# Kernel tuning notes

Measured on AMD Instinct MI355X. Metric: run time of the kernel, lower is better.

## Reference

```python
import jax, jax.numpy as jnp
import numpy as np

NR_EMB = 1024
B_COMMITMENT = 1.0


def setup_inputs() -> dict:
    key = jax.random.key(0)
    k1, k2 = jax.random.split(key)
    inpt = jax.random.normal(k1, (64, 2048, 64), dtype=jnp.float32)
    # VarianceScaling(uniform) over shape (D, K): limit = sqrt(3*scale/fan_in), scale=1, fan_in=D
    D = 64
    limit = np.sqrt(3.0 / D).astype(np.float32)
    emb_mtrx = jax.random.uniform(k2, (D, NR_EMB), dtype=jnp.float32, minval=-limit, maxval=limit)
    return {"inpt": inpt, "emb_mtrx": emb_mtrx}


def reference(inpt, emb_mtrx):
    D = inpt.shape[-1]
    x = inpt.reshape(-1, D)  # [N, D]
    dist = (jnp.sum(x * x, axis=1, keepdims=True)
            - 2.0 * (x @ emb_mtrx)
            + jnp.sum(emb_mtrx * emb_mtrx, axis=0, keepdims=True))
    idx = jnp.argmax(-dist, axis=1)  # [N]
    # avg_probs = mean of one-hot over N == normalized histogram (same math, no N x K one-hot)
    avg_probs = jnp.bincount(idx, length=NR_EMB).astype(inpt.dtype) / x.shape[0]
    perplexity = jnp.exp(-jnp.sum(avg_probs * jnp.log(avg_probs + 1e-10)))
    idx_nd = idx.reshape(inpt.shape[:-1])  # [B, T]
    q = jnp.take(emb_mtrx.T, idx_nd, axis=0)  # gather codebook rows -> [B, T, D]
    l_commitment = jnp.mean((jax.lax.stop_gradient(q) - inpt) ** 2)
    l_codebook = jnp.mean((q - jax.lax.stop_gradient(inpt)) ** 2)
    loss = B_COMMITMENT * l_commitment + l_codebook
    q = inpt + jax.lax.stop_gradient(q - inpt)  # straight-through estimator
    return q, loss, perplexity
```

## Files before the change

kernel.cpp:

```cpp
#include <hip/hip_runtime.h>

#define NROWS 131072
#define D 64
#define K 1024

typedef __attribute__((ext_vector_type(8))) short short8;
typedef __attribute__((ext_vector_type(4))) float f32x4;
typedef unsigned int u32;


__device__ __forceinline__ unsigned short f2bf_rne(float f) {
    u32 u = __float_as_uint(f);
    u += 0x7fff + ((u >> 16) & 1);
    return (unsigned short)(u >> 16);
}

__global__ __launch_bounds__(256) void prep_kernel(const float* __restrict__ E,
                                                   unsigned short* __restrict__ ehT,
                                                   float* __restrict__ e2g,
                                                   int* __restrict__ hist) {
    const int k = blockIdx.x * 256 + threadIdx.x;
    float s = 0.f;
#pragma unroll
    for (int db = 0; db < 8; ++db) {
        short8 h8;
#pragma unroll
        for (int j = 0; j < 8; ++j) {
            float v = E[(db * 8 + j) * K + k];
            s = fmaf(v, v, s);
            h8[j] = (short)f2bf_rne(v);
        }
        *(short8*)(ehT + (size_t)k * D + db * 8) = h8;
    }
    e2g[k] = -0.5f * s;
    hist[k] = 0;
}

__global__ __launch_bounds__(256, 4) void score_kernel(const float* __restrict__ X,
                                                       const unsigned short* __restrict__ ehT,
                                                       const float* __restrict__ e2g,
                                                       int* __restrict__ hist,
                                                       float* __restrict__ wavesum,
                                                       float* __restrict__ q) {
    __shared__ unsigned short ehs[2][128 * 64];
    __shared__ float e2s[2][128];
    __shared__ int idxs[4][32];

    const int tid = threadIdx.x;
    const int wave = tid >> 6;
    const int lane = tid & 63;
    const int quad = lane >> 4;
    const int lc = lane & 15;
    const size_t row0 = (size_t)blockIdx.x * 128 + wave * 32;

    u32 gofs[4];
    const u32 slotbase = wave * 256 + lane;
#pragma unroll
    for (int i = 0; i < 4; ++i) {
        u32 slot = slotbase + i * 64;
        u32 t = slot >> 7, o = (slot >> 4) & 7, ls = slot & 15;
        gofs[i] = (t * 16 + ls) * 128 + o * 16;
    }

#pragma unroll
    for (int i = 0; i < 4; ++i)
        __builtin_amdgcn_global_load_lds(
            (const __attribute__((address_space(1))) u32*)((const char*)ehT + gofs[i]),
            (__attribute__((address_space(3))) u32*)((char*)&ehs[0][0] + wave * 4096 + i * 1024),
            16, 0, 0);
    if (tid < 128) e2s[0][tid] = e2g[tid];

    short8 ax[2][2];
#pragma unroll
    for (int s = 0; s < 2; ++s) {
        const float* xr = X + (row0 + s * 16 + lc) * D + quad * 8;
#pragma unroll
        for (int ks = 0; ks < 2; ++ks) {
            float4 a = *(const float4*)(xr + ks * 32);
            float4 b = *(const float4*)(xr + ks * 32 + 4);
            union { u32 u[4]; short8 v; } pk;
            pk.u[0] = __builtin_amdgcn_perm(__float_as_uint(a.y), __float_as_uint(a.x), 0x07060302);
            pk.u[1] = __builtin_amdgcn_perm(__float_as_uint(a.w), __float_as_uint(a.z), 0x07060302);
            pk.u[2] = __builtin_amdgcn_perm(__float_as_uint(b.y), __float_as_uint(b.x), 0x07060302);
            pk.u[3] = __builtin_amdgcn_perm(__float_as_uint(b.w), __float_as_uint(b.z), 0x07060302);
            ax[s][ks] = pk.v;
        }
    }

    float best[2][4];
#pragma unroll
    for (int s = 0; s < 2; ++s)
#pragma unroll
        for (int r = 0; r < 4; ++r) best[s][r] = -3.4e38f;

    const int roff0 = quad * 256 + lc * 16;

    for (int p = 0; p < 8; ++p) {
        const int cur = p & 1;
        __syncthreads();
        if (p < 7) {
            const int nxt = (p + 1) & 1;
            const u32 gbase = (u32)(p + 1) * 16384;
#pragma unroll
            for (int i = 0; i < 4; ++i)
                __builtin_amdgcn_global_load_lds(
                    (const __attribute__((address_space(1))) u32*)((const char*)ehT + gbase + gofs[i]),
                    (__attribute__((address_space(3))) u32*)((char*)&ehs[nxt][0] + wave * 4096 + i * 1024),
                    16, 0, 0);
            if (tid < 128) e2s[nxt][tid] = e2g[(p + 1) * 128 + tid];
        }
        const char* bb = (const char*)&ehs[cur][0];
#pragma unroll 2
        for (int t = 0; t < 8; ++t) {
            short8 eb0 = *(const short8*)(bb + t * 2048 + roff0);
            short8 eb1 = *(const short8*)(bb + t * 2048 + 1024 + roff0);
            float ce2 = e2s[cur][t * 16 + lc];
            u32 cb = (u32)(p * 128 + t * 16 + lc);
#pragma unroll
            for (int s = 0; s < 2; ++s) {
                f32x4 acc = {ce2, ce2, ce2, ce2};
                acc = __builtin_amdgcn_mfma_f32_16x16x32_bf16(ax[s][0], eb0, acc, 0, 0, 0);
                acc = __builtin_amdgcn_mfma_f32_16x16x32_bf16(ax[s][1], eb1, acc, 0, 0, 0);
#pragma unroll
                for (int r = 0; r < 4; ++r) {
                    float pkv = __uint_as_float((__float_as_uint(acc[r]) & 0xFFFFFC00u) | cb);
                    best[s][r] = fmaxf(best[s][r], pkv);
                }
            }
        }
    }

#pragma unroll
    for (int off = 1; off <= 8; off <<= 1)
#pragma unroll
        for (int s = 0; s < 2; ++s)
#pragma unroll
            for (int r = 0; r < 4; ++r)
                best[s][r] = fmaxf(best[s][r], __shfl_xor(best[s][r], off, 64));

    if (lc == 0) {
#pragma unroll
        for (int s = 0; s < 2; ++s)
#pragma unroll
            for (int r = 0; r < 4; ++r)
                idxs[wave][s * 16 + quad * 4 + r] = (int)(__float_as_uint(best[s][r]) & 1023u);
    }
    if (lane < 32) atomicAdd(&hist[idxs[wave][lane]], 1);

    float ls = 0.f;
#pragma unroll 4
    for (int it = 0; it < 8; ++it) {
        int rl = it * 4 + quad;
        int k = idxs[wave][rl];
        size_t row = row0 + rl;
        float4 xv = *(const float4*)(X + row * D + lc * 4);
        short4 ev = *(const short4*)((const char*)ehT + (size_t)k * 128 + lc * 8);
        float e0 = __uint_as_float(((u32)(unsigned short)ev.x) << 16);
        float e1 = __uint_as_float(((u32)(unsigned short)ev.y) << 16);
        float e2 = __uint_as_float(((u32)(unsigned short)ev.z) << 16);
        float e3 = __uint_as_float(((u32)(unsigned short)ev.w) << 16);
        float4 o;
        float dx = e0 - xv.x; ls = fmaf(dx, dx, ls); o.x = xv.x + dx;
        float dy = e1 - xv.y; ls = fmaf(dy, dy, ls); o.y = xv.y + dy;
        float dz = e2 - xv.z; ls = fmaf(dz, dz, ls); o.z = xv.z + dz;
        float dw = e3 - xv.w; ls = fmaf(dw, dw, ls); o.w = xv.w + dw;
        *(float4*)(q + row * D + lc * 4) = o;
    }
    for (int off = 32; off > 0; off >>= 1) ls += __shfl_down(ls, off, 64);
    if (lane == 0) wavesum[blockIdx.x * 4 + wave] = ls;
}

__global__ __launch_bounds__(1024) void finalize_kernel(const int* __restrict__ hist,
                                                        const float* __restrict__ wavesum,
                                                        float* __restrict__ out) {
    __shared__ float redH[16], redL[16];
    int tid = threadIdx.x;
    float p = (float)hist[tid] * (1.0f / (float)NROWS);
    float term = p * logf(p + 1e-10f);
    float ls = wavesum[tid] + wavesum[tid + 1024] + wavesum[tid + 2048] + wavesum[tid + 3072];
    for (int off = 32; off > 0; off >>= 1) {
        term += __shfl_down(term, off, 64);
        ls += __shfl_down(ls, off, 64);
    }
    int lane = tid & 63, wid = tid >> 6;
    if (lane == 0) { redH[wid] = term; redL[wid] = ls; }
    __syncthreads();
    if (tid == 0) {
        float H = 0.f, L = 0.f;
#pragma unroll
        for (int i = 0; i < 16; ++i) { H += redH[i]; L += redL[i]; }
        out[(size_t)NROWS * D + 0] = 2.0f * (L / (float)(NROWS * D));
        out[(size_t)NROWS * D + 1] = expf(-H);
    }
}

extern "C" void kernel_launch(void* const* d_in, const int* in_sizes, int n_in,
                              void* d_out, int out_size, void* d_ws, size_t ws_size,
                              hipStream_t stream) {
    const float* X = (const float*)d_in[0];
    const float* E = (const float*)d_in[1];
    float* out = (float*)d_out;

    char* w = (char*)d_ws;
    unsigned short* ehT = (unsigned short*)(w + 0);
    float* e2g          = (float*)(w + 131072);
    int* hist           = (int*)(w + 135168);
    float* wavesum      = (float*)(w + 139264);

    prep_kernel<<<4, 256, 0, stream>>>(E, ehT, e2g, hist);
    score_kernel<<<NROWS / 128, 256, 0, stream>>>(X, ehT, e2g, hist, wavesum, out);
    finalize_kernel<<<1, 1024, 0, stream>>>(hist, wavesum, out);
}
```

Before: 134.5 us.

## Keep codebook stationary in registers and stream input rows through LDS

The score kernel is restructured so each of 16 waves in a 1024-thread block holds a 64-entry slice of the bf16 codebook and its norms in registers. Each 512-row block streams input rows in 128-row chunks through double-buffered LDS as bf16. Per-wave partial argmax values are merged across waves through shared memory before the histogram atomics. This removes the repeated per-block streaming of the whole codebook into LDS. In exchange it adds two block-wide barriers per chunk and a serial 16-way merge done by 128 threads, and it launches only 256 large blocks.

```diff
diff --git a/kernel.cpp b/kernel.cpp
--- a/kernel.cpp
+++ b/kernel.cpp
@@ -36,125 +36,109 @@
     hist[k] = 0;
 }
 
-__global__ __launch_bounds__(256, 4) void score_kernel(const float* __restrict__ X,
-                                                       const unsigned short* __restrict__ ehT,
-                                                       const float* __restrict__ e2g,
-                                                       int* __restrict__ hist,
-                                                       float* __restrict__ wavesum,
-                                                       float* __restrict__ q) {
-    __shared__ unsigned short ehs[2][128 * 64];
-    __shared__ float e2s[2][128];
-    __shared__ int idxs[4][32];
+__global__ __launch_bounds__(1024) void score_kernel(const float* __restrict__ X,
+                                                     const unsigned short* __restrict__ ehT,
+                                                     const float* __restrict__ e2g,
+                                                     int* __restrict__ hist,
+                                                     float* __restrict__ wavesum,
+                                                     float* __restrict__ q) {
+    __shared__ unsigned short xbuf[2][8192];
+    __shared__ float mrg[128 * 17];
+    __shared__ int idxl[512];
 
     const int tid = threadIdx.x;
     const int wave = tid >> 6;
     const int lane = tid & 63;
     const int quad = lane >> 4;
     const int lc = lane & 15;
-    const size_t row0 = (size_t)blockIdx.x * 128 + wave * 32;
+    const size_t row0 = (size_t)blockIdx.x * 512;
 
-    u32 gofs[4];
-    const u32 slotbase = wave * 256 + lane;
+    const int cbase = wave * 64;
+    short8 ae[4][2];
+    f32x4 e2f[4];
+    u32 cb4[4];
 #pragma unroll
-    for (int i = 0; i < 4; ++i) {
-        u32 slot = slotbase + i * 64;
-        u32 t = slot >> 7, o = (slot >> 4) & 7, ls = slot & 15;
-        gofs[i] = (t * 16 + ls) * 128 + o * 16;
+    for (int ct = 0; ct < 4; ++ct) {
+        const unsigned short* ap = ehT + ((size_t)(cbase + ct * 16 + lc) << 6) + quad * 8;
+        ae[ct][0] = *(const short8*)(ap);
+        ae[ct][1] = *(const short8*)(ap + 32);
+        e2f[ct] = *(const f32x4*)(e2g + cbase + ct * 16 + quad * 4);
+        cb4[ct] = (u32)(cbase + ct * 16 + quad * 4);
     }
 
+    const int st = tid >> 7, so = (tid >> 4) & 7, sl = tid & 15;
+    const float* sbase = X + (row0 + (size_t)(st * 16 + sl)) * D + so * 8;
+
+    float4 La = *(const float4*)(sbase);
+    float4 Lb = *(const float4*)(sbase + 4);
+    {
+        union { u32 u[4]; short8 v; } pk;
+        pk.u[0] = __builtin_amdgcn_perm(__float_as_uint(La.y), __float_as_uint(La.x), 0x07060302);
+        pk.u[1] = __builtin_amdgcn_perm(__float_as_uint(La.w), __float_as_uint(La.z), 0x07060302);
+        pk.u[2] = __builtin_amdgcn_perm(__float_as_uint(Lb.y), __float_as_uint(Lb.x), 0x07060302);
+        pk.u[3] = __builtin_amdgcn_perm(__float_as_uint(Lb.w), __float_as_uint(Lb.z), 0x07060302);
+        *(short8*)((char*)&xbuf[0][0] + tid * 16) = pk.v;
+    }
+    __syncthreads();
+
+    for (int c = 0; c < 4; ++c) {
+        const int cur = c & 1;
+        if (c < 3) {
+            La = *(const float4*)(sbase + (c + 1) * 8192);
+            Lb = *(const float4*)(sbase + (c + 1) * 8192 + 4);
+        }
+
+        const char* bb = (const char*)&xbuf[cur][0];
+#pragma unroll 2
+        for (int t = 0; t < 8; ++t) {
+            const char* bp = bb + t * 2048 + quad * 256 + lc * 16;
+            short8 b0 = *(const short8*)(bp);
+            short8 b1 = *(const short8*)(bp + 1024);
+            float bt = -3.4e38f;
 #pragma unroll
-    for (int i = 0; i < 4; ++i)
-        __builtin_amdgcn_global_load_lds(
-            (const __attribute__((address_space(1))) u32*)((const char*)ehT + gofs[i]),
-            (__attribute__((address_space(3))) u32*)((char*)&ehs[0][0] + wave * 4096 + i * 1024),
-            16, 0, 0);
-    if (tid < 128) e2s[0][tid] = e2g[tid];
+            for (int ct = 0; ct < 4; ++ct) {
+                f32x4 acc = __builtin_amdgcn_mfma_f32_16x16x32_bf16(ae[ct][0], b0, e2f[ct], 0, 0, 0);
+                acc = __builtin_amdgcn_mfma_f32_16x16x32_bf16(ae[ct][1], b1, acc, 0, 0, 0);
+#pragma unroll
+                for (int r = 0; r < 4; ++r) {
+                    float pkv = __uint_as_float((__float_as_uint(acc[r]) & 0xFFFFFC00u) | (cb4[ct] + r));
+                    bt = fmaxf(bt, pkv);
+                }
+            }
+            bt = fmaxf(bt, __shfl_xor(bt, 16, 64));
+            bt = fmaxf(bt, __shfl_xor(bt, 32, 64));
+            if (lane < 16) mrg[(t * 16 + lane) * 17 + wave] = bt;
+        }
+        __syncthreads();
 
-    short8 ax[2][2];
+        if (tid < 128) {
+            float m = mrg[tid * 17];
 #pragma unroll
-    for (int s = 0; s < 2; ++s) {
-        const float* xr = X + (row0 + s * 16 + lc) * D + quad * 8;
-#pragma unroll
-        for (int ks = 0; ks < 2; ++ks) {
-            float4 a = *(const float4*)(xr + ks * 32);
-            float4 b = *(const float4*)(xr + ks * 32 + 4);
+            for (int w = 1; w < 16; ++w) m = fmaxf(m, mrg[tid * 17 + w]);
+            int kk = (int)(__float_as_uint(m) & 1023u);
+            idxl[c * 128 + tid] = kk;
+            atomicAdd(&hist[kk], 1);
+        }
+        if (c < 3) {
             union { u32 u[4]; short8 v; } pk;
-            pk.u[0] = __builtin_amdgcn_perm(__float_as_uint(a.y), __float_as_uint(a.x), 0x07060302);
-            pk.u[1] = __builtin_amdgcn_perm(__float_as_uint(a.w), __float_as_uint(a.z), 0x07060302);
-            pk.u[2] = __builtin_amdgcn_perm(__float_as_uint(b.y), __float_as_uint(b.x), 0x07060302);
-            pk.u[3] = __builtin_amdgcn_perm(__float_as_uint(b.w), __float_as_uint(b.z), 0x07060302);
-            ax[s][ks] = pk.v;
+            pk.u[0] = __builtin_amdgcn_perm(__float_as_uint(La.y), __float_as_uint(La.x), 0x07060302);
+            pk.u[1] = __builtin_amdgcn_perm(__float_as_uint(La.w), __float_as_uint(La.z), 0x07060302);
+            pk.u[2] = __builtin_amdgcn_perm(__float_as_uint(Lb.y), __float_as_uint(Lb.x), 0x07060302);
+            pk.u[3] = __builtin_amdgcn_perm(__float_as_uint(Lb.w), __float_as_uint(Lb.z), 0x07060302);
+            *(short8*)((char*)&xbuf[cur ^ 1][0] + tid * 16) = pk.v;
         }
+        __syncthreads();
     }
 
-    float best[2][4];
-#pragma unroll
-    for (int s = 0; s < 2; ++s)
-#pragma unroll
-        for (int r = 0; r < 4; ++r) best[s][r] = -3.4e38f;
-
-    const int roff0 = quad * 256 + lc * 16;
-
-    for (int p = 0; p < 8; ++p) {
-        const int cur = p & 1;
-        __syncthreads();
-        if (p < 7) {
-            const int nxt = (p + 1) & 1;
-            const u32 gbase = (u32)(p + 1) * 16384;
-#pragma unroll
-            for (int i = 0; i < 4; ++i)
-                __builtin_amdgcn_global_load_lds(
-                    (const __attribute__((address_space(1))) u32*)((const char*)ehT + gbase + gofs[i]),
-                    (__attribute__((address_space(3))) u32*)((char*)&ehs[nxt][0] + wave * 4096 + i * 1024),
-                    16, 0, 0);
-            if (tid < 128) e2s[nxt][tid] = e2g[(p + 1) * 128 + tid];
-        }
-        const char* bb = (const char*)&ehs[cur][0];
+    float ls = 0.f;
+    const int er = tid >> 4, el = tid & 15;
 #pragma unroll 2
-        for (int t = 0; t < 8; ++t) {
-            short8 eb0 = *(const short8*)(bb + t * 2048 + roff0);
-            short8 eb1 = *(const short8*)(bb + t * 2048 + 1024 + roff0);
-            float ce2 = e2s[cur][t * 16 + lc];
-            u32 cb = (u32)(p * 128 + t * 16 + lc);
-#pragma unroll
-            for (int s = 0; s < 2; ++s) {
-                f32x4 acc = {ce2, ce2, ce2, ce2};
-                acc = __builtin_amdgcn_mfma_f32_16x16x32_bf16(ax[s][0], eb0, acc, 0, 0, 0);
-                acc = __builtin_amdgcn_mfma_f32_16x16x32_bf16(ax[s][1], eb1, acc, 0, 0, 0);
-#pragma unroll
-                for (int r = 0; r < 4; ++r) {
-                    float pkv = __uint_as_float((__float_as_uint(acc[r]) & 0xFFFFFC00u) | cb);
-                    best[s][r] = fmaxf(best[s][r], pkv);
-                }
-            }
-        }
-    }
-
-#pragma unroll
-    for (int off = 1; off <= 8; off <<= 1)
-#pragma unroll
-        for (int s = 0; s < 2; ++s)
-#pragma unroll
-            for (int r = 0; r < 4; ++r)
-                best[s][r] = fmaxf(best[s][r], __shfl_xor(best[s][r], off, 64));
-
-    if (lc == 0) {
-#pragma unroll
-        for (int s = 0; s < 2; ++s)
-#pragma unroll
-            for (int r = 0; r < 4; ++r)
-                idxs[wave][s * 16 + quad * 4 + r] = (int)(__float_as_uint(best[s][r]) & 1023u);
-    }
-    if (lane < 32) atomicAdd(&hist[idxs[wave][lane]], 1);
-
-    float ls = 0.f;
-#pragma unroll 4
     for (int it = 0; it < 8; ++it) {
-        int rl = it * 4 + quad;
-        int k = idxs[wave][rl];
+        int rl = it * 64 + er;
+        int k = idxl[rl];
         size_t row = row0 + rl;
-        float4 xv = *(const float4*)(X + row * D + lc * 4);
-        short4 ev = *(const short4*)((const char*)ehT + (size_t)k * 128 + lc * 8);
+        float4 xv = *(const float4*)(X + row * D + el * 4);
+        short4 ev = *(const short4*)((const char*)ehT + (size_t)k * 128 + el * 8);
         float e0 = __uint_as_float(((u32)(unsigned short)ev.x) << 16);
         float e1 = __uint_as_float(((u32)(unsigned short)ev.y) << 16);
         float e2 = __uint_as_float(((u32)(unsigned short)ev.z) << 16);
@@ -164,10 +148,10 @@
         float dy = e1 - xv.y; ls = fmaf(dy, dy, ls); o.y = xv.y + dy;
         float dz = e2 - xv.z; ls = fmaf(dz, dz, ls); o.z = xv.z + dz;
         float dw = e3 - xv.w; ls = fmaf(dw, dw, ls); o.w = xv.w + dw;
-        *(float4*)(q + row * D + lc * 4) = o;
+        *(float4*)(q + row * D + el * 4) = o;
     }
     for (int off = 32; off > 0; off >>= 1) ls += __shfl_down(ls, off, 64);
-    if (lane == 0) wavesum[blockIdx.x * 4 + wave] = ls;
+    if (lane == 0) wavesum[blockIdx.x * 16 + wave] = ls;
 }
 
 __global__ __launch_bounds__(1024) void finalize_kernel(const int* __restrict__ hist,
@@ -208,6 +192,6 @@
     float* wavesum      = (float*)(w + 139264);
 
     prep_kernel<<<4, 256, 0, stream>>>(E, ehT, e2g, hist);
-    score_kernel<<<NROWS / 128, 256, 0, stream>>>(X, ehT, e2g, hist, wavesum, out);
+    score_kernel<<<256, 1024, 0, stream>>>(X, ehT, e2g, hist, wavesum, out);
     finalize_kernel<<<1, 1024, 0, stream>>>(hist, wavesum, out);
 }
```

Result: faster. 124.1 us (-7.7%).
